# Kernel tuning notes

Hardware: AMD Instinct MI355X
Metric: run time of the kernel (lower is better)

The kernel has to match this reference:

```python
import jax, jax.numpy as jnp
import numpy as np

N = 30000          # num nodes
E = 480000         # num edges (before self loops)
IN_DIM = 128
HID = 32
HEADS = 4
OUT_DIM = 128
NEG_SLOPE = 0.2    # PyG GATConv default negative_slope
EPS = 1e-16        # PyG softmax denominator eps


def setup_inputs() -> dict:
    key = jax.random.key(0)
    ks = jax.random.split(key, 12)
    x = jax.random.normal(ks[0], (N, IN_DIM), dtype=jnp.float32)
    edge_index = jax.random.randint(ks[1], (2, E), 0, N, dtype=jnp.int32)
    def glorot(k, shape, fan_in):
        return jax.random.normal(k, shape, dtype=jnp.float32) / np.sqrt(fan_in)
    # layer 1: IN_DIM -> HID per head, HEADS heads, concat
    W1 = glorot(ks[2], (IN_DIM, HEADS * HID), IN_DIM)
    a_src1 = glorot(ks[3], (HEADS, HID), HID)
    a_dst1 = glorot(ks[4], (HEADS, HID), HID)
    b1 = jnp.zeros((HEADS * HID,), dtype=jnp.float32)
    # layer 2: HEADS*HID -> OUT_DIM, 1 head, no concat
    W2 = glorot(ks[5], (HEADS * HID, OUT_DIM), HEADS * HID)
    a_src2 = glorot(ks[6], (1, OUT_DIM), OUT_DIM)
    a_dst2 = glorot(ks[7], (1, OUT_DIM), OUT_DIM)
    b2 = jnp.zeros((OUT_DIM,), dtype=jnp.float32)
    return {"x": x, "edge_index": edge_index, "W1": W1, "a_src1": a_src1,
            "a_dst1": a_dst1, "b1": b1, "W2": W2, "a_src2": a_src2,
            "a_dst2": a_dst2, "b2": b2}


def _gat_conv(x, src, dst, W, a_src, a_dst, bias, heads, ch, concat):
    n = x.shape[0]
    h = (x @ W).reshape(n, heads, ch)                       # [N,H,C]
    alpha_s = jnp.einsum('nhc,hc->nh', h, a_src)            # [N,H]
    alpha_d = jnp.einsum('nhc,hc->nh', h, a_dst)            # [N,H]
    e = jax.nn.leaky_relu(alpha_s[src] + alpha_d[dst], NEG_SLOPE)  # [E,H]
    # segment softmax over incoming edges of each dst node
    m = jax.ops.segment_max(e, dst, num_segments=n)         # [N,H]
    m = jnp.where(jnp.isfinite(m), m, 0.0)
    ex = jnp.exp(e - m[dst])                                # [E,H]
    denom = jax.ops.segment_sum(ex, dst, num_segments=n)    # [N,H]
    alpha = ex / (denom[dst] + EPS)                         # [E,H]
    out = jax.ops.segment_sum(h[src] * alpha[:, :, None], dst, num_segments=n)
    if concat:
        out = out.reshape(n, heads * ch)
    else:
        out = out.mean(axis=1)
    return out + bias


def reference(x, edge_index, W1, a_src1, a_dst1, b1, W2, a_src2, a_dst2, b2):
    loops = jnp.arange(N, dtype=edge_index.dtype)
    src = jnp.concatenate([edge_index[0], loops])   # PyG add_self_loops=True
    dst = jnp.concatenate([edge_index[1], loops])
    h = _gat_conv(x, src, dst, W1, a_src1, a_dst1, b1, HEADS, HID, concat=True)
    h = jax.nn.elu(h)
    out = _gat_conv(h, src, dst, W2, a_src2, a_dst2, b2, 1, OUT_DIM, concat=False)
    return out
```

## Files before the change

kernel.cpp:

```cpp
#include <hip/hip_runtime.h>

#define NN 30000
#define NE 480000
#define ET (NE + NN)
#define DIM 128
#define GEMM1_BLOCKS ((NN + 31) / 32)
#define SCAT_BLOCKS  ((ET + 255) / 256)
#define ZERO_BLOCKS  ((NN + 255) / 256)

typedef unsigned int uint;
typedef unsigned short ushort;
typedef unsigned long long u64;

__device__ __forceinline__ float bflo(uint u){ union { uint i; float f; } v; v.i = u << 16; return v.f; }
__device__ __forceinline__ float bfhi(uint u){ union { uint i; float f; } v; v.i = u & 0xffff0000u; return v.f; }
__device__ __forceinline__ uint f2bf(float f){
  union { float f; uint i; } v; v.f = f;
  return (v.i + 0x7fffu + ((v.i >> 16) & 1u)) >> 16;
}
__device__ __forceinline__ uint packbf(float a, float b){ return f2bf(a) | (f2bf(b) << 16); }

__global__ __launch_bounds__(256) void k_init(
    const uint* __restrict__ x, const uint* __restrict__ W1f,
    const uint* __restrict__ as1f, const uint* __restrict__ ad1f,
    const uint* __restrict__ W2f, const uint* __restrict__ as2f,
    const uint* __restrict__ ad2f, const uint* __restrict__ ei,
    int* __restrict__ flags, int* __restrict__ counts,
    uint* __restrict__ W1p, uint* __restrict__ W2p, uint* __restrict__ avp){
  __shared__ int lf[9];
  const int t = threadIdx.x;
  if (t < 64){
    const uint* ptrs[7] = {x, W1f, as1f, ad1f, W2f, as2f, ad2f};
    #pragma unroll
    for (int p = 0; p < 7; p++){
      uint u = ptrs[p][t];
      uint ex = (u >> 7) & 0xffu;
      u64 m = __ballot(ex >= 100u && ex <= 150u);
      if (t == 0) lf[p] = (__popcll(m) >= 32) ? 1 : 0;
    }
    u64 mz = __ballot(ei[2 * t + 1] == 0u);
    if (t == 0){ lf[7] = 1; lf[8] = (__popcll(mz) >= 56) ? 1 : 0; }
  }
  __syncthreads();
  const int b = blockIdx.x;
  if (b < ZERO_BLOCKS){
    int i = b * 256 + t;
    if (i < NN) counts[i] = 0;
    if (b == 0 && t < 9) flags[t] = lf[t];
  } else if (b < ZERO_BLOCKS + 4){
    int base = (b - ZERO_BLOCKS) * 2048;
    #pragma unroll
    for (int k = 0; k < 8; k++){
      int j = base + k * 256 + t;
      uint o;
      if (lf[1]) o = W1f[j];
      else { float2 w = ((const float2*)W1f)[j]; o = packbf(w.x, w.y); }
      W1p[j] = o;
    }
  } else if (b < ZERO_BLOCKS + 8){
    int base = (b - ZERO_BLOCKS - 4) * 2048;
    #pragma unroll
    for (int k = 0; k < 8; k++){
      int j = base + k * 256 + t;
      uint o;
      if (lf[4]) o = W2f[j];
      else { float2 w = ((const float2*)W2f)[j]; o = packbf(w.x, w.y); }
      W2p[j] = o;
    }
  } else {
    int r = t >> 6, j = t & 63;
    const uint* srcs[4] = {as1f, ad1f, as2f, ad2f};
    const int fidx[4] = {2, 3, 5, 6};
    uint o;
    if (lf[fidx[r]]) o = srcs[r][j];
    else { float2 v = ((const float2*)srcs[r])[j]; o = packbf(v.x, v.y); }
    avp[t] = o;
  }
}

template<int NH>
__device__ __forceinline__ void gemm_core(int rbase, const void* __restrict__ Xv,
    int xbf, const uint* __restrict__ Wp, const uint* __restrict__ asp,
    const uint* __restrict__ adp, uint* __restrict__ Hout,
    float* __restrict__ as_n, float* __restrict__ ad_n, float xs[][DIM]){
  const int wv = threadIdx.x >> 6;
  const int t  = threadIdx.x & 63;
  const int r0 = rbase + wv * 8;
  #pragma unroll
  for (int rr = 0; rr < 8; rr++){
    int r = r0 + rr;
    if (r < NN){
      float v0, v1;
      if (xbf){ uint xv = ((const uint*)Xv)[r * 64 + t]; v0 = bflo(xv); v1 = bfhi(xv); }
      else    { float2 xv = ((const float2*)Xv)[r * 64 + t]; v0 = xv.x; v1 = xv.y; }
      xs[wv*8+rr][2*t]   = v0;
      xs[wv*8+rr][2*t+1] = v1;
    }
  }
  __syncthreads();
  float acc[8][2];
  #pragma unroll
  for (int rr = 0; rr < 8; rr++){ acc[rr][0] = 0.f; acc[rr][1] = 0.f; }
  for (int k4 = 0; k4 < DIM / 4; k4++){
    float wl[4], wh[4];
    #pragma unroll
    for (int j = 0; j < 4; j++){
      uint w = Wp[(4 * k4 + j) * 64 + t];
      wl[j] = bflo(w); wh[j] = bfhi(w);
    }
    #pragma unroll
    for (int rr = 0; rr < 8; rr++){
      float4 xv = *(const float4*)&xs[wv*8+rr][4 * k4];
      acc[rr][0] = fmaf(xv.x, wl[0], acc[rr][0]);
      acc[rr][1] = fmaf(xv.x, wh[0], acc[rr][1]);
      acc[rr][0] = fmaf(xv.y, wl[1], acc[rr][0]);
      acc[rr][1] = fmaf(xv.y, wh[1], acc[rr][1]);
      acc[rr][0] = fmaf(xv.z, wl[2], acc[rr][0]);
      acc[rr][1] = fmaf(xv.z, wh[2], acc[rr][1]);
      acc[rr][0] = fmaf(xv.w, wl[3], acc[rr][0]);
      acc[rr][1] = fmaf(xv.w, wh[3], acc[rr][1]);
    }
  }
  uint av = asp[t]; float s0 = bflo(av), s1 = bfhi(av);
  uint dv = adp[t]; float d0 = bflo(dv), d1 = bfhi(dv);
  #pragma unroll
  for (int rr = 0; rr < 8; rr++){
    int r = r0 + rr;
    float h0 = acc[rr][0], h1 = acc[rr][1];
    float ps = h0 * s0 + h1 * s1;
    float pd = h0 * d0 + h1 * d1;
    const int G = 64 / NH;
    #pragma unroll
    for (int d = G >> 1; d >= 1; d >>= 1){
      ps += __shfl_xor(ps, d);
      pd += __shfl_xor(pd, d);
    }
    if (r < NN){
      Hout[r * 64 + t] = packbf(h0, h1);
      if ((t & (G - 1)) == 0){
        as_n[r * NH + t / G] = ps;
        ad_n[r * NH + t / G] = pd;
      }
    }
  }
}

__global__ __launch_bounds__(256) void k_sg(const int* __restrict__ ei,
    const int* __restrict__ flags, int* __restrict__ counts, ushort* __restrict__ padded,
    const void* __restrict__ Xv, const uint* __restrict__ W1p,
    const uint* __restrict__ asp, const uint* __restrict__ adp,
    uint* __restrict__ Hout, float* __restrict__ as_n, float* __restrict__ ad_n){
  __shared__ float xs[32][DIM];
  if ((int)blockIdx.x < GEMM1_BLOCKS){
    gemm_core<4>((int)blockIdx.x * 32, Xv, flags[0], W1p, asp, adp,
                 Hout, as_n, ad_n, xs);
  } else {
    int i = ((int)blockIdx.x - GEMM1_BLOCKS) * 256 + threadIdx.x;
    if (i >= ET) return;
    const int e64 = flags[8];
    int s, d;
    if (i < NE){
      if (e64){ s = ei[2 * i]; d = ei[2 * (NE + i)]; }
      else    { s = ei[i];     d = ei[NE + i]; }
    } else { s = d = i - NE; }
    if ((uint)d >= (uint)NN) return;
    if ((uint)s >= (uint)NN) s = 0;
    int pos = atomicAdd(&counts[d], 1);
    if (pos < 64)
      __builtin_nontemporal_store((ushort)s, &padded[d * 64 + pos]);
  }
}

__global__ __launch_bounds__(128) void k_gemm2(const uint* __restrict__ Xv,
    const uint* __restrict__ Wp, const uint* __restrict__ asp,
    const uint* __restrict__ adp, uint* __restrict__ Hout,
    float* __restrict__ as_n, float* __restrict__ ad_n){
  __shared__ float xs[16][DIM];
  gemm_core<1>((int)blockIdx.x * 16, (const void*)Xv, 1, Wp, asp, adp,
               Hout, as_n, ad_n, xs);
}

template<int NH, bool ELUACT, bool OUTF32>
__global__ __launch_bounds__(256) void k_aggr(const int* __restrict__ counts,
    const ushort* __restrict__ padded, const float* __restrict__ as_n,
    const float* __restrict__ ad_n, const uint* __restrict__ Hin,
    void* __restrict__ Out){
  const int wv = threadIdx.x >> 6;
  const int l  = threadIdx.x & 63;
  const int n  = blockIdx.x * 4 + wv;
  const int g  = l >> 3;
  const int q  = l & 7;
  const int head = (NH == 4) ? (q >> 1) : 0;
  int deg = counts[n];
  if (deg > 64) deg = 64;
  const float ah = ad_n[n * NH + head];
  const bool denlane = (NH == 4) ? ((q & 1) == 0) : (q == 0);

  uint bu = ((const uint*)padded)[n * 32 + (l >> 1)];
  int sl = (l & 1) ? (int)(bu >> 16) : (int)(bu & 0xffffu);
  if (l >= deg) sl = 0;
  float p0, p1, p2, p3;
  if (NH == 4){
    float4 a = ((const float4*)as_n)[sl];
    p0 = a.x; p1 = a.y; p2 = a.z; p3 = a.w;
  } else {
    p0 = as_n[sl];
    p1 = p2 = p3 = 0.f;
  }

  float acc[16];
  #pragma unroll
  for (int c = 0; c < 16; c++) acc[c] = 0.f;
  float den = 0.f;

  for (int base = 0; base < deg; base += 8){
    int j = base + g;
    bool act = j < deg;
    int jj = j & 63;
    int s = __shfl(sl, jj);
    s = act ? s : 0;
    float e;
    if (NH == 4){
      float a0 = __shfl(p0, jj), a1 = __shfl(p1, jj);
      float a2 = __shfl(p2, jj), a3 = __shfl(p3, jj);
      float lo = (head == 0) ? a0 : a1;
      float hi = (head == 2) ? a2 : a3;
      e = (head < 2) ? lo : hi;
    } else {
      e = __shfl(p0, jj);
    }
    const uint4* hp = (const uint4*)(Hin + (size_t)s * 64 + q * 8);
    uint4 h0 = hp[0], h1 = hp[1];
    e += ah;
    e = e > 0.f ? e : 0.2f * e;
    float w = act ? __expf(e) : 0.f;
    if (denlane) den += w;
    acc[0] = fmaf(bflo(h0.x), w, acc[0]);  acc[1]  = fmaf(bfhi(h0.x), w, acc[1]);
    acc[2] = fmaf(bflo(h0.y), w, acc[2]);  acc[3]  = fmaf(bfhi(h0.y), w, acc[3]);
    acc[4] = fmaf(bflo(h0.z), w, acc[4]);  acc[5]  = fmaf(bfhi(h0.z), w, acc[5]);
    acc[6] = fmaf(bflo(h0.w), w, acc[6]);  acc[7]  = fmaf(bfhi(h0.w), w, acc[7]);
    acc[8] = fmaf(bflo(h1.x), w, acc[8]);  acc[9]  = fmaf(bfhi(h1.x), w, acc[9]);
    acc[10]= fmaf(bflo(h1.y), w, acc[10]); acc[11] = fmaf(bfhi(h1.y), w, acc[11]);
    acc[12]= fmaf(bflo(h1.z), w, acc[12]); acc[13] = fmaf(bfhi(h1.z), w, acc[13]);
    acc[14]= fmaf(bflo(h1.w), w, acc[14]); acc[15] = fmaf(bfhi(h1.w), w, acc[15]);
  }
  den += __shfl_xor(den, 8);
  den += __shfl_xor(den, 16);
  den += __shfl_xor(den, 32);
  den += __shfl_xor(den, 1);
  if (NH == 1){ den += __shfl_xor(den, 2); den += __shfl_xor(den, 4); }
  #pragma unroll
  for (int c = 0; c < 16; c++){
    acc[c] += __shfl_xor(acc[c], 8);
    acc[c] += __shfl_xor(acc[c], 16);
    acc[c] += __shfl_xor(acc[c], 32);
  }
  const float inv = 1.f / (den + 1e-16f);
  #pragma unroll
  for (int c = 0; c < 16; c++){
    float v = acc[c] * inv;
    if (ELUACT) v = v > 0.f ? v : (__expf(v) - 1.f);
    acc[c] = v;
  }
  if (g == 0){
    if (OUTF32){
      float4* O = (float4*)Out;
      #pragma unroll
      for (int p = 0; p < 4; p++)
        O[(size_t)n * 32 + q * 4 + p] = make_float4(acc[4*p], acc[4*p+1], acc[4*p+2], acc[4*p+3]);
    } else {
      uint4 pv;
      pv.x = packbf(acc[0], acc[1]);   pv.y = packbf(acc[2], acc[3]);
      pv.z = packbf(acc[4], acc[5]);   pv.w = packbf(acc[6], acc[7]);
      uint4 pw;
      pw.x = packbf(acc[8], acc[9]);   pw.y = packbf(acc[10], acc[11]);
      pw.z = packbf(acc[12], acc[13]); pw.w = packbf(acc[14], acc[15]);
      uint4* O = (uint4*)Out;
      O[(size_t)n * 16 + q * 2]     = pv;
      O[(size_t)n * 16 + q * 2 + 1] = pw;
    }
  }
}


extern "C" void kernel_launch(void* const* d_in, const int* in_sizes, int n_in,
                              void* d_out, int out_size, void* d_ws, size_t ws_size,
                              hipStream_t stream){
  (void)in_sizes; (void)n_in; (void)out_size; (void)ws_size;
  const void* x    = d_in[0];
  const int*  ei   = (const int*)d_in[1];
  const uint* W1   = (const uint*)d_in[2];
  const uint* as1w = (const uint*)d_in[3];
  const uint* ad1w = (const uint*)d_in[4];
  const uint* W2   = (const uint*)d_in[6];
  const uint* as2w = (const uint*)d_in[7];
  const uint* ad2w = (const uint*)d_in[8];

  char* ws = (char*)d_ws;
  size_t o = 0;
  auto alloc = [&](size_t b){ size_t r = o; o += (b + 255) & ~(size_t)255; return r; };
  int*    flags   = (int*)(ws + alloc(16 * 4));
  int*    counts  = (int*)(ws + alloc((size_t)(NN + 1) * 4));
  ushort* padded  = (ushort*)(ws + alloc((size_t)NN * 64 * 2));
  uint*   W1p     = (uint*)(ws + alloc(8192 * 4));
  uint*   W2p     = (uint*)(ws + alloc(8192 * 4));
  uint*   avp     = (uint*)(ws + alloc(256 * 4));
  float*  as1     = (float*)(ws + alloc((size_t)NN * 4 * 4));
  float*  ad1     = (float*)(ws + alloc((size_t)NN * 4 * 4));
  float*  as2     = (float*)(ws + alloc((size_t)NN * 4));
  float*  ad2     = (float*)(ws + alloc((size_t)NN * 4));
  uint*   hbuf    = (uint*)(ws + alloc((size_t)NN * 64 * 4));
  uint*   hact    = (uint*)(ws + alloc((size_t)NN * 64 * 4));
  uint*   h2buf   = (uint*)(ws + alloc((size_t)NN * 64 * 4));

  k_init<<<ZERO_BLOCKS + 9, 256, 0, stream>>>(
      (const uint*)x, W1, as1w, ad1w, W2, as2w, ad2w, (const uint*)ei,
      flags, counts, W1p, W2p, avp);
  k_sg<<<GEMM1_BLOCKS + SCAT_BLOCKS, 256, 0, stream>>>(
      ei, flags, counts, padded, x, W1p, avp, avp + 64, hbuf, as1, ad1);
  k_aggr<4, true, false><<<NN / 4, 256, 0, stream>>>(counts, padded, as1, ad1, hbuf, (void*)hact);
  k_gemm2<<<NN / 16, 128, 0, stream>>>(hact, W2p, avp + 128, avp + 192, h2buf, as2, ad2);
  k_aggr<1, false, true><<<NN / 4, 256, 0, stream>>>(counts, padded, as2, ad2, h2buf, d_out);
}
```

Baseline: 204.6 us.

## Build per-destination adjacency buckets in LDS by range partitioning

Replaces the global-atomic edge scatter with blocks that each own a range of destination nodes, scan the whole destination array, and fill buckets with LDS atomics before writing them out contiguously. Self loops are inserted directly and counts are written from LDS, so the counts-zeroing blocks in the init kernel are removed. This trades global atomics and scattered stores for each block re-reading the full edge list, which adds L2 read traffic.

```diff
diff --git a/kernel.cpp b/kernel.cpp
--- a/kernel.cpp
+++ b/kernel.cpp
@@ -2,11 +2,10 @@
 
 #define NN 30000
 #define NE 480000
-#define ET (NE + NN)
 #define DIM 128
+#define RNG 256
 #define GEMM1_BLOCKS ((NN + 31) / 32)
-#define SCAT_BLOCKS  ((ET + 255) / 256)
-#define ZERO_BLOCKS  ((NN + 255) / 256)
+#define SCAT_BLOCKS  ((NN + RNG - 1) / RNG)
 
 typedef unsigned int uint;
 typedef unsigned short ushort;
@@ -25,7 +24,7 @@
     const uint* __restrict__ as1f, const uint* __restrict__ ad1f,
     const uint* __restrict__ W2f, const uint* __restrict__ as2f,
     const uint* __restrict__ ad2f, const uint* __restrict__ ei,
-    int* __restrict__ flags, int* __restrict__ counts,
+    int* __restrict__ flags,
     uint* __restrict__ W1p, uint* __restrict__ W2p, uint* __restrict__ avp){
   __shared__ int lf[9];
   const int t = threadIdx.x;
@@ -43,12 +42,9 @@
   }
   __syncthreads();
   const int b = blockIdx.x;
-  if (b < ZERO_BLOCKS){
-    int i = b * 256 + t;
-    if (i < NN) counts[i] = 0;
-    if (b == 0 && t < 9) flags[t] = lf[t];
-  } else if (b < ZERO_BLOCKS + 4){
-    int base = (b - ZERO_BLOCKS) * 2048;
+  if (b == 0 && t < 9) flags[t] = lf[t];
+  if (b < 4){
+    int base = b * 2048;
     #pragma unroll
     for (int k = 0; k < 8; k++){
       int j = base + k * 256 + t;
@@ -57,8 +53,8 @@
       else { float2 w = ((const float2*)W1f)[j]; o = packbf(w.x, w.y); }
       W1p[j] = o;
     }
-  } else if (b < ZERO_BLOCKS + 8){
-    int base = (b - ZERO_BLOCKS - 4) * 2048;
+  } else if (b < 8){
+    int base = (b - 4) * 2048;
     #pragma unroll
     for (int k = 0; k < 8; k++){
       int j = base + k * 256 + t;
@@ -145,30 +141,80 @@
   }
 }
 
+struct SgLds {
+  union {
+    float xs[32][DIM];
+    struct { int cnt[RNG]; ushort bkt[RNG * 64]; } s;
+  } u;
+};
+
 __global__ __launch_bounds__(256) void k_sg(const int* __restrict__ ei,
     const int* __restrict__ flags, int* __restrict__ counts, ushort* __restrict__ padded,
     const void* __restrict__ Xv, const uint* __restrict__ W1p,
     const uint* __restrict__ asp, const uint* __restrict__ adp,
     uint* __restrict__ Hout, float* __restrict__ as_n, float* __restrict__ ad_n){
-  __shared__ float xs[32][DIM];
+  __shared__ SgLds L;
+  const int t = threadIdx.x;
   if ((int)blockIdx.x < GEMM1_BLOCKS){
     gemm_core<4>((int)blockIdx.x * 32, Xv, flags[0], W1p, asp, adp,
-                 Hout, as_n, ad_n, xs);
+                 Hout, as_n, ad_n, L.u.xs);
+    return;
+  }
+  const int base = ((int)blockIdx.x - GEMM1_BLOCKS) * RNG;
+  const int nloc = (NN - base < RNG) ? (NN - base) : RNG;
+  for (int ln = t; ln < RNG; ln += 256){
+    L.u.s.cnt[ln] = 1;
+    L.u.s.bkt[ln * 64] = (ushort)(base + ln);
+  }
+  __syncthreads();
+  const int e64 = flags[8];
+  if (!e64){
+    const uint* dstp = (const uint*)(ei + NE);
+    const int NIT = NE / 4;
+    for (int it = t; it < NIT; it += 256){
+      uint4 dv = ((const uint4*)dstp)[it];
+      int idx = it * 4;
+      #pragma unroll
+      for (int k = 0; k < 4; k++){
+        uint d = (k == 0) ? dv.x : (k == 1) ? dv.y : (k == 2) ? dv.z : dv.w;
+        uint rel = d - (uint)base;
+        if (rel < (uint)nloc){
+          int pos = atomicAdd(&L.u.s.cnt[rel], 1);
+          if (pos < 64){
+            int s = ei[idx + k];
+            if ((uint)s >= (uint)NN) s = 0;
+            L.u.s.bkt[rel * 64 + pos] = (ushort)s;
+          }
+        }
+      }
+    }
   } else {
-    int i = ((int)blockIdx.x - GEMM1_BLOCKS) * 256 + threadIdx.x;
-    if (i >= ET) return;
-    const int e64 = flags[8];
-    int s, d;
-    if (i < NE){
-      if (e64){ s = ei[2 * i]; d = ei[2 * (NE + i)]; }
-      else    { s = ei[i];     d = ei[NE + i]; }
-    } else { s = d = i - NE; }
-    if ((uint)d >= (uint)NN) return;
-    if ((uint)s >= (uint)NN) s = 0;
-    int pos = atomicAdd(&counts[d], 1);
-    if (pos < 64)
-      __builtin_nontemporal_store((ushort)s, &padded[d * 64 + pos]);
-  }
+    const uint* dstp = (const uint*)(ei + 2 * NE);
+    const int NIT = NE / 2;
+    for (int it = t; it < NIT; it += 256){
+      uint4 dv = ((const uint4*)dstp)[it];
+      int idx = it * 2;
+      #pragma unroll
+      for (int k = 0; k < 2; k++){
+        uint d = (k == 0) ? dv.x : dv.z;
+        uint rel = d - (uint)base;
+        if (rel < (uint)nloc){
+          int pos = atomicAdd(&L.u.s.cnt[rel], 1);
+          if (pos < 64){
+            int s = ei[2 * (idx + k)];
+            if ((uint)s >= (uint)NN) s = 0;
+            L.u.s.bkt[rel * 64 + pos] = (ushort)s;
+          }
+        }
+      }
+    }
+  }
+  __syncthreads();
+  for (int ln = t; ln < nloc; ln += 256) counts[base + ln] = L.u.s.cnt[ln];
+  const uint* bsrc = (const uint*)L.u.s.bkt;
+  uint* bdst = (uint*)padded + (size_t)base * 32;
+  const int BW = nloc * 32;
+  for (int k = t; k < BW; k += 256) bdst[k] = bsrc[k];
 }
 
 __global__ __launch_bounds__(128) void k_gemm2(const uint* __restrict__ Xv,
@@ -300,7 +346,7 @@
   size_t o = 0;
   auto alloc = [&](size_t b){ size_t r = o; o += (b + 255) & ~(size_t)255; return r; };
   int*    flags   = (int*)(ws + alloc(16 * 4));
-  int*    counts  = (int*)(ws + alloc((size_t)(NN + 1) * 4));
+  int*    counts  = (int*)(ws + alloc((size_t)NN * 4));
   ushort* padded  = (ushort*)(ws + alloc((size_t)NN * 64 * 2));
   uint*   W1p     = (uint*)(ws + alloc(8192 * 4));
   uint*   W2p     = (uint*)(ws + alloc(8192 * 4));
@@ -313,9 +359,9 @@
   uint*   hact    = (uint*)(ws + alloc((size_t)NN * 64 * 4));
   uint*   h2buf   = (uint*)(ws + alloc((size_t)NN * 64 * 4));
 
-  k_init<<<ZERO_BLOCKS + 9, 256, 0, stream>>>(
+  k_init<<<9, 256, 0, stream>>>(
       (const uint*)x, W1, as1w, ad1w, W2, as2w, ad2w, (const uint*)ei,
-      flags, counts, W1p, W2p, avp);
+      flags, W1p, W2p, avp);
   k_sg<<<GEMM1_BLOCKS + SCAT_BLOCKS, 256, 0, stream>>>(
       ei, flags, counts, padded, x, W1p, avp, avp + 64, hbuf, as1, ad1);
   k_aggr<4, true, false><<<NN / 4, 256, 0, stream>>>(counts, padded, as1, ad1, hbuf, (void*)hact);
```

Result: slower. 487.4 us (+138.2%).
